# Kernel optimization log

Measured on AMD Instinct MI355X. Metric: run time of the kernel, lower is better.

The kernel has to match this reference:

```python
import jax, jax.numpy as jnp
import numpy as np

FP8_MAX = 448.0  # torch.finfo(torch.float8_e4m3fn).max

def per_tensor_quantize(t):
    amax = jnp.max(jnp.abs(t))
    scale = FP8_MAX / jnp.maximum(amax, 1e-12)
    q = jnp.clip(t * scale, -FP8_MAX, FP8_MAX).astype(jnp.float8_e4m3fn)
    return q, (1.0 / scale).astype(jnp.float32)

def fp8_gemm(q, a_scale, w_q, w_scale, out_dtype):
    # emulate: linear(A.to(out)*a_scale, B.to(out)*b_scale)
    A = q.astype(out_dtype) * a_scale
    B = w_q.astype(out_dtype) * w_scale
    return A @ B.T

def setup_inputs() -> dict:
    key = jax.random.key(0)
    k1, k2, k3, k4 = jax.random.split(key, 4)
    tokens, hidden, ffn = 4096, 4096, 10752
    return {
        "x": jax.random.normal(k1, (tokens, hidden), jnp.float32),
        "expert_w1": jax.random.normal(k2, (ffn, hidden), jnp.float32) * 0.02,
        "expert_v1": jax.random.normal(k3, (ffn, hidden), jnp.float32) * 0.02,
        "expert_w2": jax.random.normal(k4, (ffn, hidden), jnp.float32) * 0.02,
    }

def reference(x, expert_w1, expert_v1, expert_w2):
    dt = x.dtype
    # weight quantization (as done in _quantize_weights per expert)
    w1_q, w1_s = per_tensor_quantize(expert_w1)
    v1_q, v1_s = per_tensor_quantize(expert_v1)
    w2_q, w2_s = per_tensor_quantize(expert_w2)
    # activation quantization + gate/up GEMMs
    qin, x_s = per_tensor_quantize(x)
    gate = fp8_gemm(qin, x_s, w1_q, w1_s, dt)          # [N, ffn]
    up = fp8_gemm(qin, x_s, v1_q, v1_s, dt)            # [N, ffn]
    inter = jax.nn.silu(gate) * up                      # fused GLU
    qmid, m_s = per_tensor_quantize(inter)
    # down proj uses expert_w2.t() -> B = [hidden, ffn]
    down = fp8_gemm(qmid, m_s, w2_q.T, w2_s, dt)        # [N, hidden]
    return down
```

## Files before the change

kernel.cpp:

```cpp
#include <hip/hip_runtime.h>
#include <cstdint>
#include <cstddef>

typedef float f32x4 __attribute__((ext_vector_type(4)));
typedef float f32x16 __attribute__((ext_vector_type(16)));
typedef int i32x4 __attribute__((ext_vector_type(4)));
typedef int i32x8 __attribute__((ext_vector_type(8)));
typedef unsigned char u8;
typedef unsigned short u16;
typedef u16 u16x8 __attribute__((ext_vector_type(8)));
typedef unsigned int u32;
typedef u32 u32x4 __attribute__((ext_vector_type(4)));

static __device__ __forceinline__ void gload_lds16(const void* g, void* l) {
  __builtin_amdgcn_global_load_lds(
      (__attribute__((address_space(1))) void*)(void*)g,
      (__attribute__((address_space(3))) void*)l,
      16, 0, 0);
}

#if defined(__has_builtin)
#if __has_builtin(__builtin_amdgcn_cvt_pk_fp8_f32)
#define HAVE_HW_FP8 1
#endif
#endif

__device__ __forceinline__ u8 f32_to_e4m3_sw(float x) {
  unsigned s = (__float_as_uint(x) >> 24) & 0x80;
  float ax = fabsf(x);
  if (!(ax > 0.0f)) return (u8)s;
  if (ax >= 448.0f) return (u8)(s | 0x7e);
  if (ax < 0.015625f) {
    int m = (int)rintf(ax * 512.0f);
    if (m >= 8) return (u8)(s | 0x08);
    return (u8)(s | m);
  }
  int e = ilogbf(ax);
  int m = (int)rintf(ldexpf(ax, 3 - e));
  if (m == 16) { ++e; m = 8; }
  return (u8)(s | ((e + 7) << 3) | (m - 8));
}

__device__ __forceinline__ unsigned cvt4_fp8(float a, float b, float c, float d) {
#ifdef HAVE_HW_FP8
  int lo = __builtin_amdgcn_cvt_pk_fp8_f32(a, b, 0, false);
  return (unsigned)__builtin_amdgcn_cvt_pk_fp8_f32(c, d, lo, true);
#else
  return (unsigned)f32_to_e4m3_sw(a) | ((unsigned)f32_to_e4m3_sw(b) << 8) |
         ((unsigned)f32_to_e4m3_sw(c) << 16) | ((unsigned)f32_to_e4m3_sw(d) << 24);
#endif
}

__device__ __forceinline__ float clamp448(float x) {
  return fminf(fmaxf(x, -448.f), 448.f);
}

__device__ __forceinline__ u16 f32_to_bf16(float x) {
  unsigned u = __float_as_uint(x);
  return (u16)((u + 0x7FFFu + ((u >> 16) & 1u)) >> 16);
}

__global__ __launch_bounds__(256) void amax4_kernel(const float* __restrict__ x,
                                                    const float* __restrict__ w1,
                                                    const float* __restrict__ v1,
                                                    const float* __restrict__ w2,
                                                    unsigned* __restrict__ out) {
  const size_t nX = (size_t)4096 * 4096 / 4;
  const size_t nW = (size_t)10752 * 4096 / 4;
  int b = (int)blockIdx.x;
  const f32x4* p;
  size_t n4;
  int slot, b0, nb;
  if (b < 232)       { p = (const f32x4*)x;  n4 = nX; slot = 0; b0 = 0;    nb = 232; }
  else if (b < 840)  { p = (const f32x4*)w1; n4 = nW; slot = 1; b0 = 232;  nb = 608; }
  else if (b < 1448) { p = (const f32x4*)v1; n4 = nW; slot = 2; b0 = 840;  nb = 608; }
  else               { p = (const f32x4*)w2; n4 = nW; slot = 3; b0 = 1448; nb = 600; }
  float m = 0.0f;
  size_t stride = (size_t)nb * 256;
  for (size_t i = (size_t)(b - b0) * 256 + threadIdx.x; i < n4; i += stride) {
    f32x4 v = p[i];
    m = fmaxf(m, fmaxf(fmaxf(fabsf(v[0]), fabsf(v[1])), fmaxf(fabsf(v[2]), fabsf(v[3]))));
  }
#pragma unroll
  for (int off = 32; off > 0; off >>= 1) m = fmaxf(m, __shfl_down(m, off));
  __shared__ float red[4];
  int lane = threadIdx.x & 63, wid = threadIdx.x >> 6;
  if (lane == 0) red[wid] = m;
  __syncthreads();
  if (threadIdx.x == 0) {
    float v = fmaxf(fmaxf(red[0], red[1]), fmaxf(red[2], red[3]));
    atomicMax(out + slot, __float_as_uint(v));
  }
}

__global__ __launch_bounds__(256) void quant2_kernel(const float* __restrict__ w1,
                                                     u8* __restrict__ w1q,
                                                     const float* __restrict__ v1,
                                                     u8* __restrict__ v1q,
                                                     const unsigned* __restrict__ scal,
                                                     size_t n8) {
  int b = (int)blockIdx.x;
  const f32x4* p;
  uint2* q;
  float amax;
  int rb;
  if (b < 1024) { p = (const f32x4*)w1; q = (uint2*)w1q; amax = __uint_as_float(scal[1]); rb = b; }
  else          { p = (const f32x4*)v1; q = (uint2*)v1q; amax = __uint_as_float(scal[2]); rb = b - 1024; }
  float scale = 448.0f / fmaxf(amax, 1e-12f);
  size_t stride = (size_t)1024 * 256;
  for (size_t i = (size_t)rb * 256 + threadIdx.x; i < n8; i += stride) {
    f32x4 a = p[2 * i], c = p[2 * i + 1];
    uint2 r;
    r.x = cvt4_fp8(clamp448(a[0] * scale), clamp448(a[1] * scale),
                   clamp448(a[2] * scale), clamp448(a[3] * scale));
    r.y = cvt4_fp8(clamp448(c[0] * scale), clamp448(c[1] * scale),
                   clamp448(c[2] * scale), clamp448(c[3] * scale));
    q[i] = r;
  }
}

__global__ __launch_bounds__(256) void pack_f32_kernel(const float* __restrict__ src,
                                                       u8* __restrict__ dst,
                                                       const unsigned* __restrict__ amax_bits,
                                                       int K) {
  float amax = __uint_as_float(*amax_bits);
  float scale = 448.0f / fmaxf(amax, 1e-12f);
  int c = (int)blockIdx.x * 256 + (int)threadIdx.x;
  int m = c & 4095;
  int kb = c >> 12;
  const f32x4* s = (const f32x4*)(src + (size_t)m * K + kb * 32);
  unsigned w[8];
#pragma unroll
  for (int j = 0; j < 8; ++j) {
    f32x4 v = s[j];
    w[j] = cvt4_fp8(clamp448(v[0] * scale), clamp448(v[1] * scale),
                    clamp448(v[2] * scale), clamp448(v[3] * scale));
  }
  u32x4* d = (u32x4*)(dst + ((size_t)kb * 4096 + m) * 32);
  d[0] = u32x4{w[0], w[1], w[2], w[3]};
  d[1] = u32x4{w[4], w[5], w[6], w[7]};
}

__global__ __launch_bounds__(256) void pack_bf16_kernel(const u16* __restrict__ src,
                                                        u8* __restrict__ dst,
                                                        const unsigned* __restrict__ amax_bits,
                                                        int K) {
  float amax = __uint_as_float(*amax_bits);
  float scale = 448.0f / fmaxf(amax, 1e-12f);
  int c = (int)blockIdx.x * 256 + (int)threadIdx.x;
  int m = c & 4095;
  int kb = c >> 12;
  const u16x8* s = (const u16x8*)(src + (size_t)m * K + kb * 32);
  unsigned w[8];
#pragma unroll
  for (int j = 0; j < 4; ++j) {
    u16x8 v = s[j];
    float f0 = __uint_as_float((unsigned)v[0] << 16) * scale;
    float f1 = __uint_as_float((unsigned)v[1] << 16) * scale;
    float f2 = __uint_as_float((unsigned)v[2] << 16) * scale;
    float f3 = __uint_as_float((unsigned)v[3] << 16) * scale;
    float f4 = __uint_as_float((unsigned)v[4] << 16) * scale;
    float f5 = __uint_as_float((unsigned)v[5] << 16) * scale;
    float f6 = __uint_as_float((unsigned)v[6] << 16) * scale;
    float f7 = __uint_as_float((unsigned)v[7] << 16) * scale;
    w[2 * j]     = cvt4_fp8(clamp448(f0), clamp448(f1), clamp448(f2), clamp448(f3));
    w[2 * j + 1] = cvt4_fp8(clamp448(f4), clamp448(f5), clamp448(f6), clamp448(f7));
  }
  u32x4* d = (u32x4*)(dst + ((size_t)kb * 4096 + m) * 32);
  d[0] = u32x4{w[0], w[1], w[2], w[3]};
  d[1] = u32x4{w[4], w[5], w[6], w[7]};
}

__global__ __launch_bounds__(256) void quantT_kernel(const float* __restrict__ src,
                                                     u8* __restrict__ dst,
                                                     const unsigned* __restrict__ amax_bits,
                                                     int R, int C) {
  __shared__ float t[64][65];
  float amax = __uint_as_float(*amax_bits);
  float scale = 448.0f / fmaxf(amax, 1e-12f);
  int nbr = R >> 6;
  int br = (int)blockIdx.x % nbr, bc = (int)blockIdx.x / nbr;
  int r0 = br * 64, c0 = bc * 64;
  int tid = threadIdx.x;
  int lc = tid & 63, lr = tid >> 6;
#pragma unroll
  for (int i = 0; i < 16; ++i)
    t[lr + i * 4][lc] = src[(size_t)(r0 + lr + i * 4) * C + c0 + lc];
  __syncthreads();
  int qd = tid & 15, xbase = tid >> 4;
#pragma unroll
  for (int i = 0; i < 4; ++i) {
    int x = xbase + 16 * i;
    float v0 = clamp448(t[4 * qd + 0][x] * scale);
    float v1 = clamp448(t[4 * qd + 1][x] * scale);
    float v2 = clamp448(t[4 * qd + 2][x] * scale);
    float v3 = clamp448(t[4 * qd + 3][x] * scale);
    *(unsigned*)(dst + (size_t)(c0 + x) * R + r0 + 4 * qd) = cvt4_fp8(v0, v1, v2, v3);
  }
}

__device__ __forceinline__ int swz_key(int r) { return (r >> 2) & 3; }

__device__ __forceinline__ int swz_off32(int r, int h) {
  return r * 64 + ((((h << 1) ^ swz_key(r)) << 4));
}

__device__ __forceinline__ i32x8 ld_frag(const u8* base, int r, int h) {
  int o = swz_off32(r, h);
  i32x8 f;
  f.lo = *(const i32x4*)(base + o);
  f.hi = *(const i32x4*)(base + (o ^ 16));
  return f;
}

__device__ __forceinline__ i32x8 ld_a_g(const u8* p) {
  i32x8 f;
  f.lo = *(const i32x4*)p;
  f.hi = *(const i32x4*)(p + 16);
  return f;
}

#define MFMA_MX(a, b, c) \
  __builtin_amdgcn_mfma_scale_f32_32x32x64_f8f6f4((a), (b), (c), 0, 0, 0, 0x7F7F7F7F, 0, 0x7F7F7F7F)

__global__ __launch_bounds__(256, 2) void gemm1_gateup(
    const u8* __restrict__ Apk, const u8* __restrict__ Wq, const u8* __restrict__ Vq,
    const unsigned* __restrict__ scal, u16* __restrict__ inter,
    unsigned* __restrict__ amax_mid, int M, int N, int K) {
  __shared__ __align__(16) u8 lW[3][8192], lV[3][8192];
  __shared__ float red[4];
  int tid = threadIdx.x;
  int lane = tid & 63, wid = tid >> 6;
  int wm = wid >> 1, wn = wid & 1;

  int bid = (int)blockIdx.x;
  int bm = bid & 31;
  int bn = bid >> 5;

  int r0 = tid >> 2;
  int kblk = ((tid & 3) ^ swz_key(r0)) << 4;
  const u8* wS = Wq + (size_t)(bn * 128 + r0) * K + kblk;
  const u8* vS = Vq + (size_t)(bn * 128 + r0) * K + kblk;
  size_t rK = (size_t)64 * K;

  f32x16 g00 = (f32x16)(0.f), g01 = (f32x16)(0.f), g10 = (f32x16)(0.f), g11 = (f32x16)(0.f);
  f32x16 u00 = (f32x16)(0.f), u01 = (f32x16)(0.f), u10 = (f32x16)(0.f), u11 = (f32x16)(0.f);

  int rfrag = lane & 31;
  int h = lane >> 5;
  int arow = wm * 64 + rfrag;
  int brow = wn * 64 + rfrag;

  const size_t tStride = (size_t)64 * M;
  const u8* aP = Apk + 32 * ((size_t)M * h + (size_t)(bm * 128 + arow));

  int NT = K >> 6;
  {
    gload_lds16(wS + 0, lW[0] + tid * 16);
    gload_lds16(wS + 0 + rK, lW[0] + 4096 + tid * 16);
    gload_lds16(vS + 0, lV[0] + tid * 16);
    gload_lds16(vS + 0 + rK, lV[0] + 4096 + tid * 16);
    gload_lds16(wS + 64, lW[1] + tid * 16);
    gload_lds16(wS + 64 + rK, lW[1] + 4096 + tid * 16);
    gload_lds16(vS + 64, lV[1] + tid * 16);
    gload_lds16(vS + 64 + rK, lV[1] + 4096 + tid * 16);
  }
  i32x8 ac0 = ld_a_g(aP);
  i32x8 ac1 = ld_a_g(aP + 1024);
  i32x8 an0 = ac0, an1 = ac1;

  for (int t = 0; t < NT; ++t) {
    int cur = t % 3;
    int nx = cur + 2; if (nx >= 3) nx -= 3;
    int kt2 = (t + 2) * 64;
    bool do_stage = (t + 2) < NT;
    bool do_pref = (t + 1) < NT;
    if (do_pref) {
      asm volatile("s_waitcnt vmcnt(8)" ::: "memory");
    } else {
      asm volatile("s_waitcnt vmcnt(0)" ::: "memory");
    }
    __builtin_amdgcn_s_barrier();
    i32x8 w0 = ld_frag(lW[cur], brow, h);
    i32x8 w1 = ld_frag(lW[cur], brow + 32, h);
    i32x8 v0 = ld_frag(lV[cur], brow, h);
    i32x8 v1 = ld_frag(lV[cur], brow + 32, h);
    if (do_pref) {
      const u8* ap = aP + (size_t)(t + 1) * tStride;
      an0 = ld_a_g(ap);
      an1 = ld_a_g(ap + 1024);
    }
    if (do_stage) {
      gload_lds16(wS + kt2, lW[nx] + tid * 16);
      gload_lds16(wS + kt2 + rK, lW[nx] + 4096 + tid * 16);
      gload_lds16(vS + kt2, lV[nx] + tid * 16);
      gload_lds16(vS + kt2 + rK, lV[nx] + 4096 + tid * 16);
    }
    __builtin_amdgcn_s_barrier();
    __builtin_amdgcn_s_setprio(1);
    g00 = MFMA_MX(ac0, w0, g00);
    g10 = MFMA_MX(ac1, w0, g10);
    g01 = MFMA_MX(ac0, w1, g01);
    g11 = MFMA_MX(ac1, w1, g11);
    u00 = MFMA_MX(ac0, v0, u00);
    u10 = MFMA_MX(ac1, v0, u10);
    u01 = MFMA_MX(ac0, v1, u01);
    u11 = MFMA_MX(ac1, v1, u11);
    __builtin_amdgcn_s_setprio(0);
    ac0 = an0; ac1 = an1;
  }

  float ax = __uint_as_float(scal[0]);
  float aw = __uint_as_float(scal[1]);
  float av = __uint_as_float(scal[2]);
  float inv_x = 1.0f / (448.0f / fmaxf(ax, 1e-12f));
  float inv_w = 1.0f / (448.0f / fmaxf(aw, 1e-12f));
  float inv_v = 1.0f / (448.0f / fmaxf(av, 1e-12f));
  float sg = inv_x * inv_w, su = inv_x * inv_v;

  int rb = bm * 128 + wm * 64 + h * 4;
  int cb = bn * 128 + wn * 64 + rfrag;
  float lmax = 0.0f;
#pragma unroll
  for (int mi = 0; mi < 2; ++mi)
#pragma unroll
    for (int ni = 0; ni < 2; ++ni) {
      const f32x16& gg = mi ? (ni ? g11 : g10) : (ni ? g01 : g00);
      const f32x16& uu = mi ? (ni ? u11 : u10) : (ni ? u01 : u00);
#pragma unroll
      for (int q = 0; q < 16; ++q) {
        int rr = rb + mi * 32 + (q & 3) + 8 * (q >> 2);
        float gv = gg[q] * sg;
        float uv = uu[q] * su;
        float iv = gv / (1.0f + expf(-gv)) * uv;
        inter[(size_t)rr * N + (cb + ni * 32)] = f32_to_bf16(iv);
        lmax = fmaxf(lmax, fabsf(iv));
      }
    }
#pragma unroll
  for (int off = 32; off > 0; off >>= 1) lmax = fmaxf(lmax, __shfl_down(lmax, off));
  if (lane == 0) red[wid] = lmax;
  __syncthreads();
  if (tid == 0)
    atomicMax(amax_mid, __float_as_uint(fmaxf(fmaxf(red[0], red[1]), fmaxf(red[2], red[3]))));
}

__global__ __launch_bounds__(256, 2) void gemm2_down(
    const u8* __restrict__ Apk, const u8* __restrict__ Bq,
    const unsigned* __restrict__ amax_a, const unsigned* __restrict__ amax_b,
    float* __restrict__ out, int M, int N, int K) {
  __shared__ __align__(16) u8 lB[3][8192];
  int tid = threadIdx.x;
  int lane = tid & 63, wid = tid >> 6;
  int wm = wid >> 1, wn = wid & 1;

  int bid = (int)blockIdx.x;
  int bm = bid & 31;
  int bn = bid >> 5;

  int r0 = tid >> 2;
  int kblk = ((tid & 3) ^ swz_key(r0)) << 4;
  const u8* bS = Bq + (size_t)(bn * 128 + r0) * K + kblk;
  size_t rK = (size_t)64 * K;

  f32x16 c00 = (f32x16)(0.f), c01 = (f32x16)(0.f);
  f32x16 c10 = (f32x16)(0.f), c11 = (f32x16)(0.f);

  int rfrag = lane & 31;
  int h = lane >> 5;
  int arow = wm * 64 + rfrag;
  int brow = wn * 64 + rfrag;

  const size_t tStride = (size_t)64 * M;
  const u8* aP = Apk + 32 * ((size_t)M * h + (size_t)(bm * 128 + arow));

  int NT = K >> 6;
  {
    gload_lds16(bS + 0, lB[0] + tid * 16);
    gload_lds16(bS + 0 + rK, lB[0] + 4096 + tid * 16);
    gload_lds16(bS + 64, lB[1] + tid * 16);
    gload_lds16(bS + 64 + rK, lB[1] + 4096 + tid * 16);
  }
  i32x8 ac0 = ld_a_g(aP);
  i32x8 ac1 = ld_a_g(aP + 1024);
  i32x8 an0 = ac0, an1 = ac1;

  for (int t = 0; t < NT; ++t) {
    int cur = t % 3;
    int nx = cur + 2; if (nx >= 3) nx -= 3;
    int kt2 = (t + 2) * 64;
    bool do_stage = (t + 2) < NT;
    bool do_pref = (t + 1) < NT;
    if (do_pref) {
      asm volatile("s_waitcnt vmcnt(6)" ::: "memory");
    } else {
      asm volatile("s_waitcnt vmcnt(0)" ::: "memory");
    }
    __builtin_amdgcn_s_barrier();
    i32x8 b0 = ld_frag(lB[cur], brow, h);
    i32x8 b1 = ld_frag(lB[cur], brow + 32, h);
    if (do_pref) {
      const u8* ap = aP + (size_t)(t + 1) * tStride;
      an0 = ld_a_g(ap);
      an1 = ld_a_g(ap + 1024);
    }
    if (do_stage) {
      gload_lds16(bS + kt2, lB[nx] + tid * 16);
      gload_lds16(bS + kt2 + rK, lB[nx] + 4096 + tid * 16);
    }
    __builtin_amdgcn_s_barrier();
    __builtin_amdgcn_s_setprio(1);
    c00 = MFMA_MX(ac0, b0, c00);
    c10 = MFMA_MX(ac1, b0, c10);
    c01 = MFMA_MX(ac0, b1, c01);
    c11 = MFMA_MX(ac1, b1, c11);
    __builtin_amdgcn_s_setprio(0);
    ac0 = an0; ac1 = an1;
  }

  float sa = 1.0f / (448.0f / fmaxf(__uint_as_float(*amax_a), 1e-12f));
  float sb = 1.0f / (448.0f / fmaxf(__uint_as_float(*amax_b), 1e-12f));
  float sc = sa * sb;

  int rb = bm * 128 + wm * 64 + h * 4;
  int cb = bn * 128 + wn * 64 + rfrag;
#pragma unroll
  for (int mi = 0; mi < 2; ++mi)
#pragma unroll
    for (int ni = 0; ni < 2; ++ni) {
      const f32x16& cc = mi ? (ni ? c11 : c10) : (ni ? c01 : c00);
#pragma unroll
      for (int q = 0; q < 16; ++q) {
        int rr = rb + mi * 32 + (q & 3) + 8 * (q >> 2);
        out[(size_t)rr * N + (cb + ni * 32)] = cc[q] * sc;
      }
    }
}

extern "C" void kernel_launch(void* const* d_in, const int* in_sizes, int n_in,
                              void* d_out, int out_size, void* d_ws, size_t ws_size,
                              hipStream_t stream) {
  const float* x  = (const float*)d_in[0];
  const float* w1 = (const float*)d_in[1];
  const float* v1 = (const float*)d_in[2];
  const float* w2 = (const float*)d_in[3];
  const int M = 4096, H = 4096, F = 10752;

  u8* ws = (u8*)d_ws;
  unsigned* scal = (unsigned*)ws;
  u8* xpk  = ws + 256;
  u8* w1q  = xpk  + (size_t)M * H;
  u8* v1q  = w1q  + (size_t)F * H;
  u8* w2qT = v1q  + (size_t)F * H;
  u8* midpk = w2qT + (size_t)F * H;
  u16* inter = (u16*)(midpk + (size_t)M * F);

  hipMemsetAsync(scal, 0, 256, stream);
  amax4_kernel<<<2048, 256, 0, stream>>>(x, w1, v1, w2, scal);

  pack_f32_kernel<<<(M * (H / 32)) / 256, 256, 0, stream>>>(x, xpk, scal + 0, H);
  quant2_kernel<<<2048, 256, 0, stream>>>(w1, w1q, v1, v1q, scal, (size_t)F * H / 8);
  quantT_kernel<<<(F / 64) * (H / 64), 256, 0, stream>>>(w2, w2qT, scal + 3, F, H);

  gemm1_gateup<<<(M / 128) * (F / 128), 256, 0, stream>>>(xpk, w1q, v1q, scal, inter,
                                                          scal + 4, M, F, H);
  pack_bf16_kernel<<<(M * (F / 32)) / 256, 256, 0, stream>>>(inter, midpk, scal + 4, F);
  gemm2_down<<<(M / 128) * (H / 128), 256, 0, stream>>>(midpk, w2qT, scal + 4, scal + 3,
                                                        (float*)d_out, M, H, F);
}
```

Baseline: 975.4 us.

## Widen down-projection GEMM tile to 128x256 for more B-fragment reuse

The down-projection GEMM now gives each block 256 output columns instead of 128. Each wave keeps eight MFMA accumulators instead of four and stages four 64-row B slices per K step, with the LDS ring buffers enlarged to match and the vmcnt wait threshold raised for the extra loads. The aim is to reuse each A fragment loaded from global memory across twice as many MFMAs and to halve the grid so it fits in a single wave of blocks. The cost is more accumulator registers, more LDS per block, and fewer blocks available to hide latency.

```diff
diff --git a/kernel.cpp b/kernel.cpp
--- a/kernel.cpp
+++ b/kernel.cpp
@@ -349,7 +349,7 @@
     const u8* __restrict__ Apk, const u8* __restrict__ Bq,
     const unsigned* __restrict__ amax_a, const unsigned* __restrict__ amax_b,
     float* __restrict__ out, int M, int N, int K) {
-  __shared__ __align__(16) u8 lB[3][8192];
+  __shared__ __align__(16) u8 lB[3][16384];
   int tid = threadIdx.x;
   int lane = tid & 63, wid = tid >> 6;
   int wm = wid >> 1, wn = wid & 1;
@@ -360,27 +360,31 @@
 
   int r0 = tid >> 2;
   int kblk = ((tid & 3) ^ swz_key(r0)) << 4;
-  const u8* bS = Bq + (size_t)(bn * 128 + r0) * K + kblk;
+  const u8* bS = Bq + (size_t)(bn * 256 + r0) * K + kblk;
   size_t rK = (size_t)64 * K;
 
-  f32x16 c00 = (f32x16)(0.f), c01 = (f32x16)(0.f);
-  f32x16 c10 = (f32x16)(0.f), c11 = (f32x16)(0.f);
+  f32x16 d00 = (f32x16)(0.f), d01 = (f32x16)(0.f), d02 = (f32x16)(0.f), d03 = (f32x16)(0.f);
+  f32x16 d10 = (f32x16)(0.f), d11 = (f32x16)(0.f), d12 = (f32x16)(0.f), d13 = (f32x16)(0.f);
 
   int rfrag = lane & 31;
   int h = lane >> 5;
   int arow = wm * 64 + rfrag;
-  int brow = wn * 64 + rfrag;
+  int brow = wn * 128 + rfrag;
 
   const size_t tStride = (size_t)64 * M;
   const u8* aP = Apk + 32 * ((size_t)M * h + (size_t)(bm * 128 + arow));
 
+#define STG2(buf, off)                                             \
+  do {                                                             \
+    gload_lds16(bS + (off),          lB[buf] + tid * 16);          \
+    gload_lds16(bS + (off) + rK,     lB[buf] + 4096 + tid * 16);   \
+    gload_lds16(bS + (off) + 2 * rK, lB[buf] + 8192 + tid * 16);   \
+    gload_lds16(bS + (off) + 3 * rK, lB[buf] + 12288 + tid * 16);  \
+  } while (0)
+
   int NT = K >> 6;
-  {
-    gload_lds16(bS + 0, lB[0] + tid * 16);
-    gload_lds16(bS + 0 + rK, lB[0] + 4096 + tid * 16);
-    gload_lds16(bS + 64, lB[1] + tid * 16);
-    gload_lds16(bS + 64 + rK, lB[1] + 4096 + tid * 16);
-  }
+  STG2(0, 0);
+  STG2(1, 64);
   i32x8 ac0 = ld_a_g(aP);
   i32x8 ac1 = ld_a_g(aP + 1024);
   i32x8 an0 = ac0, an1 = ac1;
@@ -392,43 +396,48 @@
     bool do_stage = (t + 2) < NT;
     bool do_pref = (t + 1) < NT;
     if (do_pref) {
-      asm volatile("s_waitcnt vmcnt(6)" ::: "memory");
+      asm volatile("s_waitcnt vmcnt(8)" ::: "memory");
     } else {
       asm volatile("s_waitcnt vmcnt(0)" ::: "memory");
     }
     __builtin_amdgcn_s_barrier();
     i32x8 b0 = ld_frag(lB[cur], brow, h);
     i32x8 b1 = ld_frag(lB[cur], brow + 32, h);
+    i32x8 b2 = ld_frag(lB[cur], brow + 64, h);
+    i32x8 b3 = ld_frag(lB[cur], brow + 96, h);
     if (do_pref) {
       const u8* ap = aP + (size_t)(t + 1) * tStride;
       an0 = ld_a_g(ap);
       an1 = ld_a_g(ap + 1024);
     }
-    if (do_stage) {
-      gload_lds16(bS + kt2, lB[nx] + tid * 16);
-      gload_lds16(bS + kt2 + rK, lB[nx] + 4096 + tid * 16);
-    }
+    if (do_stage) STG2(nx, kt2);
     __builtin_amdgcn_s_barrier();
     __builtin_amdgcn_s_setprio(1);
-    c00 = MFMA_MX(ac0, b0, c00);
-    c10 = MFMA_MX(ac1, b0, c10);
-    c01 = MFMA_MX(ac0, b1, c01);
-    c11 = MFMA_MX(ac1, b1, c11);
+    d00 = MFMA_MX(ac0, b0, d00);
+    d10 = MFMA_MX(ac1, b0, d10);
+    d01 = MFMA_MX(ac0, b1, d01);
+    d11 = MFMA_MX(ac1, b1, d11);
+    d02 = MFMA_MX(ac0, b2, d02);
+    d12 = MFMA_MX(ac1, b2, d12);
+    d03 = MFMA_MX(ac0, b3, d03);
+    d13 = MFMA_MX(ac1, b3, d13);
     __builtin_amdgcn_s_setprio(0);
     ac0 = an0; ac1 = an1;
   }
+#undef STG2
 
   float sa = 1.0f / (448.0f / fmaxf(__uint_as_float(*amax_a), 1e-12f));
   float sb = 1.0f / (448.0f / fmaxf(__uint_as_float(*amax_b), 1e-12f));
   float sc = sa * sb;
 
   int rb = bm * 128 + wm * 64 + h * 4;
-  int cb = bn * 128 + wn * 64 + rfrag;
+  int cb = bn * 256 + wn * 128 + rfrag;
 #pragma unroll
   for (int mi = 0; mi < 2; ++mi)
 #pragma unroll
-    for (int ni = 0; ni < 2; ++ni) {
-      const f32x16& cc = mi ? (ni ? c11 : c10) : (ni ? c01 : c00);
+    for (int ni = 0; ni < 4; ++ni) {
+      const f32x16& cc = mi ? (ni == 0 ? d10 : ni == 1 ? d11 : ni == 2 ? d12 : d13)
+                            : (ni == 0 ? d00 : ni == 1 ? d01 : ni == 2 ? d02 : d03);
 #pragma unroll
       for (int q = 0; q < 16; ++q) {
         int rr = rb + mi * 32 + (q & 3) + 8 * (q >> 2);
@@ -465,6 +474,6 @@
   gemm1_gateup<<<(M / 128) * (F / 128), 256, 0, stream>>>(xpk, w1q, v1q, scal, inter,
                                                           scal + 4, M, F, H);
   pack_bf16_kernel<<<(M * (F / 32)) / 256, 256, 0, stream>>>(inter, midpk, scal + 4, F);
-  gemm2_down<<<(M / 128) * (H / 128), 256, 0, stream>>>(midpk, w2qT, scal + 4, scal + 3,
+  gemm2_down<<<(M / 128) * (H / 256), 256, 0, stream>>>(midpk, w2qT, scal + 4, scal + 3,
                                                         (float*)d_out, M, H, F);
 }
```

New measurement: 893.8 us. 8.4% less time.

## Reshape GEMM block tiles to 256 rows with more A fragments per warp

Applied to the files above, without the earlier changes.

Both GEMMs now use 256-row M tiles, with each warp holding four A fragments loaded straight from global memory into registers. The gate/up GEMM narrows the N tile to 64, so each warp reuses one W and one V fragment across four A fragments, and its LDS buffers shrink. The down GEMM keeps a 128-wide N tile, so its block tile grows to 256x128 and the grid halves. The aim is more MFMA work per LDS fragment read and fewer redundant weight loads, at the cost of more A register traffic and pressure. It also adds a full wait and barrier after the prologue.

```diff
diff --git a/kernel.cpp b/kernel.cpp
--- a/kernel.cpp
+++ b/kernel.cpp
@@ -227,47 +227,44 @@
     const u8* __restrict__ Apk, const u8* __restrict__ Wq, const u8* __restrict__ Vq,
     const unsigned* __restrict__ scal, u16* __restrict__ inter,
     unsigned* __restrict__ amax_mid, int M, int N, int K) {
-  __shared__ __align__(16) u8 lW[3][8192], lV[3][8192];
+  __shared__ __align__(16) u8 lW[3][4096], lV[3][4096];
   __shared__ float red[4];
   int tid = threadIdx.x;
   int lane = tid & 63, wid = tid >> 6;
   int wm = wid >> 1, wn = wid & 1;
 
   int bid = (int)blockIdx.x;
-  int bm = bid & 31;
-  int bn = bid >> 5;
+  int bm = bid & 15;
+  int bn = bid >> 4;
 
   int r0 = tid >> 2;
   int kblk = ((tid & 3) ^ swz_key(r0)) << 4;
-  const u8* wS = Wq + (size_t)(bn * 128 + r0) * K + kblk;
-  const u8* vS = Vq + (size_t)(bn * 128 + r0) * K + kblk;
-  size_t rK = (size_t)64 * K;
-
-  f32x16 g00 = (f32x16)(0.f), g01 = (f32x16)(0.f), g10 = (f32x16)(0.f), g11 = (f32x16)(0.f);
-  f32x16 u00 = (f32x16)(0.f), u01 = (f32x16)(0.f), u10 = (f32x16)(0.f), u11 = (f32x16)(0.f);
+  const u8* wS = Wq + (size_t)(bn * 64 + r0) * K + kblk;
+  const u8* vS = Vq + (size_t)(bn * 64 + r0) * K + kblk;
+
+  f32x16 g0 = (f32x16)(0.f), g1 = (f32x16)(0.f), g2 = (f32x16)(0.f), g3 = (f32x16)(0.f);
+  f32x16 u0 = (f32x16)(0.f), u1 = (f32x16)(0.f), u2 = (f32x16)(0.f), u3 = (f32x16)(0.f);
 
   int rfrag = lane & 31;
   int h = lane >> 5;
-  int arow = wm * 64 + rfrag;
-  int brow = wn * 64 + rfrag;
+  int arow = wm * 128 + rfrag;
+  int brow = wn * 32 + rfrag;
 
   const size_t tStride = (size_t)64 * M;
-  const u8* aP = Apk + 32 * ((size_t)M * h + (size_t)(bm * 128 + arow));
+  const u8* aP = Apk + 32 * ((size_t)M * h + (size_t)(bm * 256 + arow));
 
   int NT = K >> 6;
-  {
-    gload_lds16(wS + 0, lW[0] + tid * 16);
-    gload_lds16(wS + 0 + rK, lW[0] + 4096 + tid * 16);
-    gload_lds16(vS + 0, lV[0] + tid * 16);
-    gload_lds16(vS + 0 + rK, lV[0] + 4096 + tid * 16);
-    gload_lds16(wS + 64, lW[1] + tid * 16);
-    gload_lds16(wS + 64 + rK, lW[1] + 4096 + tid * 16);
-    gload_lds16(vS + 64, lV[1] + tid * 16);
-    gload_lds16(vS + 64 + rK, lV[1] + 4096 + tid * 16);
-  }
+  gload_lds16(wS + 0, lW[0] + tid * 16);
+  gload_lds16(vS + 0, lV[0] + tid * 16);
+  gload_lds16(wS + 64, lW[1] + tid * 16);
+  gload_lds16(vS + 64, lV[1] + tid * 16);
   i32x8 ac0 = ld_a_g(aP);
   i32x8 ac1 = ld_a_g(aP + 1024);
-  i32x8 an0 = ac0, an1 = ac1;
+  i32x8 ac2 = ld_a_g(aP + 2048);
+  i32x8 ac3 = ld_a_g(aP + 3072);
+  i32x8 an0 = ac0, an1 = ac1, an2 = ac2, an3 = ac3;
+  asm volatile("s_waitcnt vmcnt(0)" ::: "memory");
+  __builtin_amdgcn_s_barrier();
 
   for (int t = 0; t < NT; ++t) {
     int cur = t % 3;
@@ -276,38 +273,36 @@
     bool do_stage = (t + 2) < NT;
     bool do_pref = (t + 1) < NT;
     if (do_pref) {
-      asm volatile("s_waitcnt vmcnt(8)" ::: "memory");
+      asm volatile("s_waitcnt vmcnt(10)" ::: "memory");
     } else {
       asm volatile("s_waitcnt vmcnt(0)" ::: "memory");
     }
     __builtin_amdgcn_s_barrier();
     i32x8 w0 = ld_frag(lW[cur], brow, h);
-    i32x8 w1 = ld_frag(lW[cur], brow + 32, h);
     i32x8 v0 = ld_frag(lV[cur], brow, h);
-    i32x8 v1 = ld_frag(lV[cur], brow + 32, h);
     if (do_pref) {
       const u8* ap = aP + (size_t)(t + 1) * tStride;
       an0 = ld_a_g(ap);
       an1 = ld_a_g(ap + 1024);
+      an2 = ld_a_g(ap + 2048);
+      an3 = ld_a_g(ap + 3072);
     }
     if (do_stage) {
       gload_lds16(wS + kt2, lW[nx] + tid * 16);
-      gload_lds16(wS + kt2 + rK, lW[nx] + 4096 + tid * 16);
       gload_lds16(vS + kt2, lV[nx] + tid * 16);
-      gload_lds16(vS + kt2 + rK, lV[nx] + 4096 + tid * 16);
     }
     __builtin_amdgcn_s_barrier();
     __builtin_amdgcn_s_setprio(1);
-    g00 = MFMA_MX(ac0, w0, g00);
-    g10 = MFMA_MX(ac1, w0, g10);
-    g01 = MFMA_MX(ac0, w1, g01);
-    g11 = MFMA_MX(ac1, w1, g11);
-    u00 = MFMA_MX(ac0, v0, u00);
-    u10 = MFMA_MX(ac1, v0, u10);
-    u01 = MFMA_MX(ac0, v1, u01);
-    u11 = MFMA_MX(ac1, v1, u11);
+    g0 = MFMA_MX(ac0, w0, g0);
+    g1 = MFMA_MX(ac1, w0, g1);
+    g2 = MFMA_MX(ac2, w0, g2);
+    g3 = MFMA_MX(ac3, w0, g3);
+    u0 = MFMA_MX(ac0, v0, u0);
+    u1 = MFMA_MX(ac1, v0, u1);
+    u2 = MFMA_MX(ac2, v0, u2);
+    u3 = MFMA_MX(ac3, v0, u3);
     __builtin_amdgcn_s_setprio(0);
-    ac0 = an0; ac1 = an1;
+    ac0 = an0; ac1 = an1; ac2 = an2; ac3 = an3;
   }
 
   float ax = __uint_as_float(scal[0]);
@@ -318,25 +313,23 @@
   float inv_v = 1.0f / (448.0f / fmaxf(av, 1e-12f));
   float sg = inv_x * inv_w, su = inv_x * inv_v;
 
-  int rb = bm * 128 + wm * 64 + h * 4;
-  int cb = bn * 128 + wn * 64 + rfrag;
+  int rb = bm * 256 + wm * 128 + h * 4;
+  int cb = bn * 64 + wn * 32 + rfrag;
   float lmax = 0.0f;
 #pragma unroll
-  for (int mi = 0; mi < 2; ++mi)
-#pragma unroll
-    for (int ni = 0; ni < 2; ++ni) {
-      const f32x16& gg = mi ? (ni ? g11 : g10) : (ni ? g01 : g00);
-      const f32x16& uu = mi ? (ni ? u11 : u10) : (ni ? u01 : u00);
-#pragma unroll
-      for (int q = 0; q < 16; ++q) {
-        int rr = rb + mi * 32 + (q & 3) + 8 * (q >> 2);
-        float gv = gg[q] * sg;
-        float uv = uu[q] * su;
-        float iv = gv / (1.0f + expf(-gv)) * uv;
-        inter[(size_t)rr * N + (cb + ni * 32)] = f32_to_bf16(iv);
-        lmax = fmaxf(lmax, fabsf(iv));
-      }
-    }
+  for (int mi = 0; mi < 4; ++mi) {
+    const f32x16& gg = mi == 0 ? g0 : mi == 1 ? g1 : mi == 2 ? g2 : g3;
+    const f32x16& uu = mi == 0 ? u0 : mi == 1 ? u1 : mi == 2 ? u2 : u3;
+#pragma unroll
+    for (int q = 0; q < 16; ++q) {
+      int rr = rb + mi * 32 + (q & 3) + 8 * (q >> 2);
+      float gv = gg[q] * sg;
+      float uv = uu[q] * su;
+      float iv = gv / (1.0f + expf(-gv)) * uv;
+      inter[(size_t)rr * N + cb] = f32_to_bf16(iv);
+      lmax = fmaxf(lmax, fabsf(iv));
+    }
+  }
 #pragma unroll
   for (int off = 32; off > 0; off >>= 1) lmax = fmaxf(lmax, __shfl_down(lmax, off));
   if (lane == 0) red[wid] = lmax;
@@ -355,35 +348,37 @@
   int wm = wid >> 1, wn = wid & 1;
 
   int bid = (int)blockIdx.x;
-  int bm = bid & 31;
-  int bn = bid >> 5;
+  int bm = bid & 15;
+  int bn = bid >> 4;
 
   int r0 = tid >> 2;
   int kblk = ((tid & 3) ^ swz_key(r0)) << 4;
   const u8* bS = Bq + (size_t)(bn * 128 + r0) * K + kblk;
   size_t rK = (size_t)64 * K;
 
-  f32x16 c00 = (f32x16)(0.f), c01 = (f32x16)(0.f);
-  f32x16 c10 = (f32x16)(0.f), c11 = (f32x16)(0.f);
+  f32x16 d0 = (f32x16)(0.f), d1 = (f32x16)(0.f), d2 = (f32x16)(0.f), d3 = (f32x16)(0.f);
+  f32x16 e0 = (f32x16)(0.f), e1 = (f32x16)(0.f), e2 = (f32x16)(0.f), e3 = (f32x16)(0.f);
 
   int rfrag = lane & 31;
   int h = lane >> 5;
-  int arow = wm * 64 + rfrag;
+  int arow = wm * 128 + rfrag;
   int brow = wn * 64 + rfrag;
 
   const size_t tStride = (size_t)64 * M;
-  const u8* aP = Apk + 32 * ((size_t)M * h + (size_t)(bm * 128 + arow));
+  const u8* aP = Apk + 32 * ((size_t)M * h + (size_t)(bm * 256 + arow));
 
   int NT = K >> 6;
-  {
-    gload_lds16(bS + 0, lB[0] + tid * 16);
-    gload_lds16(bS + 0 + rK, lB[0] + 4096 + tid * 16);
-    gload_lds16(bS + 64, lB[1] + tid * 16);
-    gload_lds16(bS + 64 + rK, lB[1] + 4096 + tid * 16);
-  }
+  gload_lds16(bS + 0, lB[0] + tid * 16);
+  gload_lds16(bS + 0 + rK, lB[0] + 4096 + tid * 16);
+  gload_lds16(bS + 64, lB[1] + tid * 16);
+  gload_lds16(bS + 64 + rK, lB[1] + 4096 + tid * 16);
   i32x8 ac0 = ld_a_g(aP);
   i32x8 ac1 = ld_a_g(aP + 1024);
-  i32x8 an0 = ac0, an1 = ac1;
+  i32x8 ac2 = ld_a_g(aP + 2048);
+  i32x8 ac3 = ld_a_g(aP + 3072);
+  i32x8 an0 = ac0, an1 = ac1, an2 = ac2, an3 = ac3;
+  asm volatile("s_waitcnt vmcnt(0)" ::: "memory");
+  __builtin_amdgcn_s_barrier();
 
   for (int t = 0; t < NT; ++t) {
     int cur = t % 3;
@@ -392,7 +387,7 @@
     bool do_stage = (t + 2) < NT;
     bool do_pref = (t + 1) < NT;
     if (do_pref) {
-      asm volatile("s_waitcnt vmcnt(6)" ::: "memory");
+      asm volatile("s_waitcnt vmcnt(10)" ::: "memory");
     } else {
       asm volatile("s_waitcnt vmcnt(0)" ::: "memory");
     }
@@ -403,6 +398,8 @@
       const u8* ap = aP + (size_t)(t + 1) * tStride;
       an0 = ld_a_g(ap);
       an1 = ld_a_g(ap + 1024);
+      an2 = ld_a_g(ap + 2048);
+      an3 = ld_a_g(ap + 3072);
     }
     if (do_stage) {
       gload_lds16(bS + kt2, lB[nx] + tid * 16);
@@ -410,31 +407,35 @@
     }
     __builtin_amdgcn_s_barrier();
     __builtin_amdgcn_s_setprio(1);
-    c00 = MFMA_MX(ac0, b0, c00);
-    c10 = MFMA_MX(ac1, b0, c10);
-    c01 = MFMA_MX(ac0, b1, c01);
-    c11 = MFMA_MX(ac1, b1, c11);
+    d0 = MFMA_MX(ac0, b0, d0);
+    d1 = MFMA_MX(ac1, b0, d1);
+    d2 = MFMA_MX(ac2, b0, d2);
+    d3 = MFMA_MX(ac3, b0, d3);
+    e0 = MFMA_MX(ac0, b1, e0);
+    e1 = MFMA_MX(ac1, b1, e1);
+    e2 = MFMA_MX(ac2, b1, e2);
+    e3 = MFMA_MX(ac3, b1, e3);
     __builtin_amdgcn_s_setprio(0);
-    ac0 = an0; ac1 = an1;
+    ac0 = an0; ac1 = an1; ac2 = an2; ac3 = an3;
   }
 
   float sa = 1.0f / (448.0f / fmaxf(__uint_as_float(*amax_a), 1e-12f));
   float sb = 1.0f / (448.0f / fmaxf(__uint_as_float(*amax_b), 1e-12f));
   float sc = sa * sb;
 
-  int rb = bm * 128 + wm * 64 + h * 4;
+  int rb = bm * 256 + wm * 128 + h * 4;
   int cb = bn * 128 + wn * 64 + rfrag;
 #pragma unroll
-  for (int mi = 0; mi < 2; ++mi)
-#pragma unroll
-    for (int ni = 0; ni < 2; ++ni) {
-      const f32x16& cc = mi ? (ni ? c11 : c10) : (ni ? c01 : c00);
-#pragma unroll
-      for (int q = 0; q < 16; ++q) {
-        int rr = rb + mi * 32 + (q & 3) + 8 * (q >> 2);
-        out[(size_t)rr * N + (cb + ni * 32)] = cc[q] * sc;
-      }
-    }
+  for (int mi = 0; mi < 4; ++mi) {
+    const f32x16& dd = mi == 0 ? d0 : mi == 1 ? d1 : mi == 2 ? d2 : d3;
+    const f32x16& ee = mi == 0 ? e0 : mi == 1 ? e1 : mi == 2 ? e2 : e3;
+#pragma unroll
+    for (int q = 0; q < 16; ++q) {
+      int rr = rb + mi * 32 + (q & 3) + 8 * (q >> 2);
+      out[(size_t)rr * N + cb] = dd[q] * sc;
+      out[(size_t)rr * N + cb + 32] = ee[q] * sc;
+    }
+  }
 }
 
 extern "C" void kernel_launch(void* const* d_in, const int* in_sizes, int n_in,
@@ -462,9 +463,9 @@
   quant2_kernel<<<2048, 256, 0, stream>>>(w1, w1q, v1, v1q, scal, (size_t)F * H / 8);
   quantT_kernel<<<(F / 64) * (H / 64), 256, 0, stream>>>(w2, w2qT, scal + 3, F, H);
 
-  gemm1_gateup<<<(M / 128) * (F / 128), 256, 0, stream>>>(xpk, w1q, v1q, scal, inter,
-                                                          scal + 4, M, F, H);
+  gemm1_gateup<<<(M / 256) * (F / 64), 256, 0, stream>>>(xpk, w1q, v1q, scal, inter,
+                                                         scal + 4, M, F, H);
   pack_bf16_kernel<<<(M * (F / 32)) / 256, 256, 0, stream>>>(inter, midpk, scal + 4, F);
-  gemm2_down<<<(M / 128) * (H / 128), 256, 0, stream>>>(midpk, w2qT, scal + 4, scal + 3,
+  gemm2_down<<<(M / 256) * (H / 128), 256, 0, stream>>>(midpk, w2qT, scal + 4, scal + 3,
                                                         (float*)d_out, M, H, F);
 }
```

Result: faster. 888.4 us, median of 2 (-8.9%).
